# Performance work log

Hardware: AMD Instinct MI355X
Metric: run time of the kernel (lower is better)

The kernel has to match this reference:

```python
import jax, jax.numpy as jnp
import numpy as np

D_MODEL = 512; D_STATE = 64; D_CONV = 4; EXPAND = 1; HEADDIM = 128; NGROUPS = 2; CHUNK = 256
D_INNER = EXPAND * (D_MODEL // 2)          # 256
NHEADS = D_INNER // HEADDIM                 # 2
CONV_DIM = D_INNER + 2 * NGROUPS * D_STATE  # 512
D_IN_PROJ = CONV_DIM + NHEADS               # 514

def silu(x):
    return x * jax.nn.sigmoid(x)

def conv1x1(x, w, b):
    # x: (b,c,h,w), w: (o,c)
    return jnp.einsum('bchw,oc->bohw', x, w) + b[None, :, None, None]

def dwconv3x3(x, w, b):
    # depthwise 3x3, SAME padding; w: (c,1,3,3)
    c = x.shape[1]
    y = jax.lax.conv_general_dilated(x, w, (1, 1), 'SAME', feature_group_count=c,
                                     dimension_numbers=('NCHW', 'OIHW', 'NCHW'))
    return y + b[None, :, None, None]

def causal_dwconv1d(x, w, b):
    # x: (b,L,c); w: (c,k). Torch pads k-1 both sides then slices [:L] -> causal left pad.
    k = w.shape[1]
    xp = jnp.pad(x, ((0, 0), (k - 1, 0), (0, 0))).transpose(0, 2, 1)  # (b,c,L+k-1)
    y = jax.lax.conv_general_dilated(xp, w[:, None, :], (1,), 'VALID',
                                     feature_group_count=w.shape[0],
                                     dimension_numbers=('NCH', 'OIH', 'NCH'))
    return y.transpose(0, 2, 1) + b

def axis_attn(x, qw, qb, fw, fb, axis):
    # DualAxisAggAttn single-axis step
    qkv = conv1x1(x, qw, qb)
    c = x.shape[1]
    q, k, v = qkv[:, :1], qkv[:, 1:1 + c], qkv[:, 1 + c:]
    dim = -1 if axis == 'W' else -2
    scores = jax.nn.softmax(q, axis=dim)
    ctx = jnp.sum(k * scores, axis=dim, keepdims=True)
    out = x + jax.nn.sigmoid(v) * ctx
    return conv1x1(out, fw, fb)

def segsum(x):
    # x: (...,T) -> (...,T,T) lower-triangular segment sums, -inf above diagonal
    T = x.shape[-1]
    cs = jnp.cumsum(x, -1)
    d = cs[..., :, None] - cs[..., None, :]
    mask = jnp.tril(jnp.ones((T, T), bool))
    return jnp.where(mask, d, -jnp.inf)

def ssd(X, A, B, C, chunk):
    # Mamba2 SSD chunked scan. X: (b,l,h,p) = x*dt; A: (b,l,h) = dt*A_head; B,C: (b,l,h,n)
    b, l, h, p = X.shape; n = B.shape[-1]; c = l // chunk
    X = X.reshape(b, c, chunk, h, p)
    B = B.reshape(b, c, chunk, h, n)
    C = C.reshape(b, c, chunk, h, n)
    A = A.reshape(b, c, chunk, h).transpose(0, 3, 1, 2)  # (b,h,c,L)
    Acs = jnp.cumsum(A, -1)
    L = jnp.exp(segsum(A))  # (b,h,c,L,L) intra-chunk decay
    Yd = jnp.einsum('bclhn,bcshn,bhcls,bcshp->bclhp', C, B, L, X)
    dec = jnp.exp(Acs[..., -1:] - Acs)
    st = jnp.einsum('bclhn,bhcl,bclhp->bchpn', B, dec, X)  # chunk end-states
    st = jnp.concatenate([jnp.zeros_like(st[:, :1]), st], 1)
    dchunk = jnp.exp(segsum(jnp.pad(Acs[..., -1], ((0, 0), (0, 0), (1, 0)))))
    st = jnp.einsum('bhzc,bchpn->bzhpn', dchunk, st)[:, :-1]  # states entering each chunk
    Yo = jnp.einsum('bclhn,bchpn,bhcl->bclhp', C, st, jnp.exp(Acs))
    return (Yd + Yo).reshape(b, l, h, p)

def setup_inputs() -> dict:
    key = jax.random.key(0)
    ks = jax.random.split(key, 12)
    s = 0.02
    p = {}
    p['u'] = jax.random.normal(ks[0], (8, D_MODEL, 64, 64), jnp.float32)
    p['sc_w1'] = jax.random.normal(ks[1], (D_MODEL, D_MODEL)) * s
    p['sc_b1'] = jnp.zeros((D_MODEL,))
    p['sc_wdw'] = jax.random.normal(ks[2], (D_MODEL, 1, 3, 3)) * s
    p['sc_bdw'] = jnp.zeros((D_MODEL,))
    p['sc_w2'] = jax.random.normal(ks[3], (D_INNER, D_MODEL)) * s
    p['sc_b2'] = jnp.zeros((D_INNER,))
    p['mc_w'] = jax.random.normal(ks[4], (D_INNER, D_MODEL)) * s
    p['mc_b'] = jnp.zeros((D_INNER,))
    p['qkvW_w'] = jax.random.normal(ks[5], (1 + 2 * D_INNER, D_INNER)) * s
    p['qkvW_b'] = jnp.zeros((1 + 2 * D_INNER,))
    p['qkvH_w'] = jax.random.normal(ks[6], (1 + 2 * D_INNER, D_INNER)) * s
    p['qkvH_b'] = jnp.zeros((1 + 2 * D_INNER,))
    p['fuseW_w'] = jax.random.normal(ks[7], (D_INNER, D_INNER)) * s
    p['fuseW_b'] = jnp.zeros((D_INNER,))
    p['fuseH_w'] = jax.random.normal(ks[8], (D_INNER, D_INNER)) * s
    p['fuseH_b'] = jnp.zeros((D_INNER,))
    p['in_proj_w'] = jax.random.normal(ks[9], (D_IN_PROJ, D_INNER)) * s
    p['conv1d_w'] = jax.random.normal(ks[10], (CONV_DIM, D_CONV)) * s
    p['conv1d_b'] = jnp.zeros((CONV_DIM,))
    dt = np.exp(np.linspace(np.log(1e-3), np.log(0.1), NHEADS))
    p['dt_bias'] = jnp.asarray(dt + np.log(-np.expm1(-dt)), jnp.float32)
    p['A_log'] = jnp.asarray(np.log(np.linspace(1.0, 16.0, NHEADS)), jnp.float32)
    p['D'] = jnp.ones((NHEADS,))
    p['norm_w'] = jnp.ones((D_INNER,))
    p['outp_w'] = jax.random.normal(ks[11], (D_MODEL, 2 * D_INNER)) * s
    p['outp_b'] = jnp.zeros((D_MODEL,))
    return p

def reference(u, sc_w1, sc_b1, sc_wdw, sc_bdw, sc_w2, sc_b2, mc_w, mc_b,
              qkvW_w, qkvW_b, qkvH_w, qkvH_b, fuseW_w, fuseW_b, fuseH_w, fuseH_b,
              in_proj_w, conv1d_w, conv1d_b, dt_bias, A_log, D, norm_w, outp_w, outp_b):
    b, _, H, W = u.shape
    # short_conv branch (light_ConvBlock: 1x1 -> dw3x3 -> 1x1, all SiLU; BN folded into bias)
    z = silu(conv1x1(u, sc_w1, sc_b1))
    z = silu(dwconv3x3(z, sc_wdw, sc_bdw))
    z = silu(conv1x1(z, sc_w2, sc_b2))
    # main branch
    x = silu(conv1x1(u, mc_w, mc_b))
    x = axis_attn(x, qkvW_w, qkvW_b, fuseW_w, fuseW_b, 'W')
    x = axis_attn(x, qkvH_w, qkvH_b, fuseH_w, fuseH_b, 'H')
    seqlen = H * W
    u2 = x.transpose(0, 2, 3, 1).reshape(b, seqlen, D_INNER)  # b (h w) c
    xbcdt = u2 @ in_proj_w.T  # (b,l,d_in_proj)
    xBC = xbcdt[..., :CONV_DIM]
    dt = jax.nn.softplus(xbcdt[..., CONV_DIM:] + dt_bias)  # (b,l,h)
    A = -jnp.exp(A_log)  # (h,)
    xBC = silu(causal_dwconv1d(xBC, conv1d_w, conv1d_b))
    xs = xBC[..., :D_INNER]
    Bs = xBC[..., D_INNER:D_INNER + NGROUPS * D_STATE].reshape(b, seqlen, NGROUPS, D_STATE)
    Cs = xBC[..., D_INNER + NGROUPS * D_STATE:].reshape(b, seqlen, NGROUPS, D_STATE)
    Xh = xs.reshape(b, seqlen, NHEADS, HEADDIM)
    rep = NHEADS // NGROUPS
    Bh = jnp.repeat(Bs, rep, axis=2)
    Ch = jnp.repeat(Cs, rep, axis=2)
    y = ssd(Xh * dt[..., None], dt * A[None, None, :], Bh, Ch, CHUNK)
    y = y + Xh * D[None, None, :, None]  # D skip connection
    y = y.reshape(b, seqlen, D_INNER)
    # RMSNormGated with z=None -> plain RMSNorm
    y = y * jax.lax.rsqrt(jnp.mean(y * y, -1, keepdims=True) + 1e-5) * norm_w
    y = y.reshape(b, H, W, D_INNER).transpose(0, 3, 1, 2)
    y = jnp.concatenate([z, y], axis=1)
    return conv1x1(y, outp_w, outp_b)
```

## Files before the change

### kernel.cpp

```cpp
#include <hip/hip_runtime.h>
#include <hip/hip_bf16.h>
#include <cstddef>
#include <cstdint>

#define PTOT 32768
#define HWSZ 4096

typedef __attribute__((ext_vector_type(8))) short bf16x8;
typedef __attribute__((ext_vector_type(4))) short s16x4;
typedef __attribute__((ext_vector_type(4))) float f32x4;

__device__ __forceinline__ float sigf(float x){ return 1.f/(1.f+__expf(-x)); }
__device__ __forceinline__ float siluf(float x){ return x*sigf(x); }
__device__ __forceinline__ short f2b(float x){
  __hip_bfloat16 h = __float2bfloat16(x);
  return *reinterpret_cast<short*>(&h);
}
__device__ __forceinline__ float b2f(short s){
  unsigned u = ((unsigned)(unsigned short)s) << 16;
  return __uint_as_float(u);
}

__device__ __forceinline__ void gload16(const void* g, void* l){
  __builtin_amdgcn_global_load_lds(
      (const __attribute__((address_space(1))) unsigned int*)g,
      (__attribute__((address_space(3))) unsigned int*)l, 16, 0, 0);
}

__global__ __launch_bounds__(256) void k_cvtw(
    const float* __restrict__ s0, const float* __restrict__ s1, const float* __restrict__ s2,
    const float* __restrict__ s3, const float* __restrict__ s4,
    short* __restrict__ dst){
  int idx = blockIdx.x*256 + threadIdx.x;
  const float* s; int off;
  if      (idx <  262144){ s=s0; off=idx; }
  else if (idx <  393216){ s=s1; off=idx- 262144; }
  else if (idx <  524288){ s=s2; off=idx- 393216; }
  else if (idx <  655616){ s=s3; off=idx- 524288; }
  else if (idx <  917760){ s=s4; off=idx- 655616; }
  else return;
  dst[idx] = f2b(s[off]);
}

__global__ __launch_bounds__(256) void k_wcomp(
    const float* __restrict__ qkvHw, const float* __restrict__ fuWw,
    const float* __restrict__ fuWb,  const float* __restrict__ qkvHb,
    const float* __restrict__ inpw,  const float* __restrict__ fuHw,
    const float* __restrict__ fuHb,
    const float* __restrict__ scb1,  const float* __restrict__ mcb,
    short* __restrict__ wcomb, float* __restrict__ bcomb,
    short* __restrict__ wi2,   float* __restrict__ bi2,
    short* __restrict__ wqH,   short* __restrict__ wdt,
    float* __restrict__ bzx)
{
  int blk = blockIdx.x;
  int tid = threadIdx.x;
  __shared__ float as[256];
  __shared__ float red[256];
  if (blk < 513){
    int i = blk;
    int r = (i==512) ? 0 : (i+1);
    as[tid]  = qkvHw[(size_t)r*256 + tid];
    red[tid] = as[tid] * fuWb[tid];
    __syncthreads();
    for (int off=128; off; off>>=1){ if (tid<off) red[tid]+=red[tid+off]; __syncthreads(); }
    float acc = 0.f;
    #pragma unroll 8
    for (int k=0;k<256;k++) acc += as[k]*fuWw[(size_t)k*256 + tid];
    if (i < 512){
      wcomb[(size_t)(256+i)*256 + tid] = f2b(acc);
      if (tid==0) bcomb[256+i] = red[0] + qkvHb[r];
    } else {
      wqH[tid] = f2b(acc);
      if (tid==0) bcomb[768] = red[0] + qkvHb[0];
    }
  } else if (blk < 769){
    int j = blk - 513;
    wcomb[(size_t)j*256 + tid] = f2b(fuWw[(size_t)j*256 + tid]);
    if (tid==0) bcomb[j] = fuWb[j];
  } else if (blk < 1283){
    int j = blk - 769;
    as[tid]  = inpw[(size_t)j*256 + tid];
    red[tid] = as[tid] * fuHb[tid];
    __syncthreads();
    for (int off=128; off; off>>=1){ if (tid<off) red[tid]+=red[tid+off]; __syncthreads(); }
    float acc = 0.f;
    #pragma unroll 8
    for (int k=0;k<256;k++) acc += as[k]*fuHw[(size_t)k*256 + tid];
    if (j < 512){
      wi2[(size_t)j*256 + tid] = f2b(acc);
      if (tid==0) bi2[j] = red[0];
    } else {
      wdt[(size_t)(j-512)*256 + tid] = f2b(acc);
      if (tid==0) bi2[j] = red[0];
    }
  } else {
    int j = (blk - 1283)*256 + tid;
    bzx[j] = (j < 512) ? scb1[j] : mcb[j-512];
  }
}

__global__ __launch_bounds__(256) void k_transpose(const float* __restrict__ in, short* __restrict__ out){
  __shared__ float tile[64][33];
  int b = blockIdx.z;
  int c0 = blockIdx.y * 64;
  int s0 = blockIdx.x * 32;
  int tx = threadIdx.x, ty = threadIdx.y;
  const float* ip = in + ((size_t)b*512 + c0)*HWSZ + s0;
  for (int i = ty; i < 64; i += 8) tile[i][tx] = ip[(size_t)i*HWSZ + tx];
  __syncthreads();
  for (int i = ty; i < 32; i += 8){
    unsigned lo = (unsigned)(unsigned short)f2b(tile[2*tx][i]);
    unsigned hi = (unsigned)(unsigned short)f2b(tile[2*tx+1][i]);
    unsigned pk = lo | (hi<<16);
    *reinterpret_cast<unsigned*>(&out[((size_t)((b<<12) + s0 + i))*512 + c0 + 2*tx]) = pk;
  }
}

template<int ACT, int OUT_NCHW>
__global__ __launch_bounds__(256) void k_gemm(
    const short* __restrict__ A0, const short* __restrict__ A1,
    int kSplit, int lda0, int lda1,
    const short* __restrict__ Wt, const float* __restrict__ bias,
    void* __restrict__ Cpv, int N, int K, int ldc, int qkvPerm,
    short* __restrict__ Cp2, int nSplit2, int ldc2)
{
  __shared__ short Alds[3][128*32];
  __shared__ short Wlds[2][128*32];

  int tid = threadIdx.x;
  int lane = tid & 63;
  int wv = tid >> 6;
  int wr = wv >> 1, wc = wv & 1;
  int lr = lane & 15, lh = lane >> 4;
  int bm = blockIdx.x * 128;
  int bn = blockIdx.y * 128;

  int rl = lane >> 2;
  int kg = (lane & 3) << 3;

  int ar[2], wnr[2];
  #pragma unroll
  for (int j=0;j<2;j++){
    int r = wv*32 + j*16 + rl;
    ar[j] = bm + r;
    int n = bn + r; if (n > N-1) n = N-1;
    wnr[j] = qkvPerm ? (n+1) : n;
  }

  auto stage_a = [&](int buf, int t){
    int k0 = t << 5;
    #pragma unroll
    for (int j=0;j<2;j++){
      const short* asrc;
      if (k0 < kSplit) asrc = A0 + (size_t)ar[j]*lda0 + (k0 + kg);
      else             asrc = A1 + (size_t)ar[j]*lda1 + (k0 - kSplit + kg);
      gload16(asrc, &Alds[buf][(wv*32 + j*16)*32]);
    }
  };
  auto stage_w = [&](int buf, int t){
    int k0 = t << 5;
    #pragma unroll
    for (int j=0;j<2;j++){
      const short* bsrc = Wt + (size_t)wnr[j]*K + (k0 + kg);
      gload16(bsrc, &Wlds[buf][(wv*32 + j*16)*32]);
    }
  };

  f32x4 acc[4][4];
  #pragma unroll
  for (int i=0;i<4;i++)
    #pragma unroll
    for (int j=0;j<4;j++) acc[i][j] = (f32x4){0.f,0.f,0.f,0.f};

  int NT = K >> 5;
  stage_w(0, 0);
  __builtin_amdgcn_sched_barrier(0);
  stage_a(0, 0);
  __builtin_amdgcn_sched_barrier(0);
  stage_a(1, 1);
  for (int t=0; t<NT; t++){
    int ab = t % 3, wb = t & 1;
    if (t+1 < NT) asm volatile("s_waitcnt vmcnt(2)" ::: "memory");
    else          asm volatile("s_waitcnt vmcnt(0)" ::: "memory");
    __builtin_amdgcn_s_barrier();
    __builtin_amdgcn_sched_barrier(0);
    if (t+1 < NT) stage_w(wb^1, t+1);
    __builtin_amdgcn_sched_barrier(0);
    if (t+2 < NT) stage_a((t+2)%3, t+2);
    __builtin_amdgcn_sched_barrier(0);
    bf16x8 af[4], bfr[4];
    #pragma unroll
    for (int mi=0;mi<4;mi++)
      af[mi] = *reinterpret_cast<const bf16x8*>(&Alds[ab][(wr*64 + mi*16 + lr)*32 + lh*8]);
    #pragma unroll
    for (int ni=0;ni<4;ni++)
      bfr[ni] = *reinterpret_cast<const bf16x8*>(&Wlds[wb][(wc*64 + ni*16 + lr)*32 + lh*8]);
    #pragma unroll
    for (int mi=0;mi<4;mi++)
      #pragma unroll
      for (int ni=0;ni<4;ni++)
        acc[mi][ni] = __builtin_amdgcn_mfma_f32_16x16x32_bf16(af[mi], bfr[ni], acc[mi][ni], 0, 0, 0);
  }

  if (!OUT_NCHW){
    short* Cp = (short*)Cpv;
    #pragma unroll
    for (int mi=0;mi<4;mi++){
      int m = bm + wr*64 + mi*16 + lh*4;
      #pragma unroll
      for (int ni=0;ni<4;ni++){
        int n = bn + wc*64 + ni*16 + lr;
        if (n < N){
          int wn = qkvPerm ? (n+1) : n;
          float bb = bias ? bias[wn] : 0.f;
          #pragma unroll
          for (int r=0;r<4;r++){
            float v = acc[mi][ni][r] + bb;
            if (ACT==1) v = siluf(v);
            short sv = f2b(v);
            if (n < nSplit2) Cp[(size_t)(m+r)*ldc + n] = sv;
            else             Cp2[(size_t)(m+r)*ldc2 + (n - nSplit2)] = sv;
          }
        }
      }
    }
  } else {
    float* Cp = (float*)Cpv;
    float* Sep = ((float*)Alds) + wv*16*68;
    #pragma unroll
    for (int mi=0;mi<4;mi++){
      __syncthreads();
      #pragma unroll
      for (int ni=0;ni<4;ni++){
        int n = bn + wc*64 + ni*16 + lr;
        float bb = (bias && n < N) ? bias[n] : 0.f;
        #pragma unroll
        for (int r=0;r<4;r++){
          float v = acc[mi][ni][r] + bb;
          if (ACT==1) v = siluf(v);
          Sep[(lh*4+r)*68 + ni*16 + lr] = v;
        }
      }
      __syncthreads();
      int m = bm + wr*64 + mi*16 + lr;
      size_t mb = ((size_t)(m>>12)*ldc)*HWSZ + (m & 4095);
      #pragma unroll
      for (int g=0; g<16; g++){
        int nl = g*4 + lh;
        float v = Sep[lr*68 + nl];
        int nn = bn + wc*64 + nl;
        if (nn < N) Cp[mb + (size_t)nn*HWSZ] = v;
      }
    }
  }
}

__global__ __launch_bounds__(256) void k_dwconv3x3(const short* __restrict__ in,
    const float* __restrict__ w, const float* __restrict__ bias, short* __restrict__ out){
  int tid = threadIdx.x;
  int cq = tid & 127;
  int wi = tid >> 7;
  int bw = blockIdx.x;
  int b  = bw >> 5;
  int wc = ((bw & 31) << 1) | wi;
  int h0 = blockIdx.y << 4;
  int c  = cq << 2;

  float arr[36];
  {
    const float* wp = &w[c*9];
    #pragma unroll
    for (int t=0;t<9;t++){
      f32x4 v = *reinterpret_cast<const f32x4*>(wp + t*4);
      arr[t*4+0]=v[0]; arr[t*4+1]=v[1]; arr[t*4+2]=v[2]; arr[t*4+3]=v[3];
    }
  }
  f32x4 bias4 = *reinterpret_cast<const f32x4*>(&bias[c]);

  int pb = b << 12;
  auto ldrow = [&](int r, int dw)->f32x4 {
    int ww = wc + dw;
    if ((unsigned)r >= 64u || (unsigned)ww >= 64u) return (f32x4){0.f,0.f,0.f,0.f};
    s16x4 v = *reinterpret_cast<const s16x4*>(&in[((size_t)(pb + (r<<6) + ww) << 9) + c]);
    return (f32x4){b2f(v[0]), b2f(v[1]), b2f(v[2]), b2f(v[3])};
  };

  f32x4 a00,a01,a02,a10,a11,a12,a20,a21,a22;
  a00=ldrow(h0-1,-1); a01=ldrow(h0-1,0); a02=ldrow(h0-1,1);
  a10=ldrow(h0  ,-1); a11=ldrow(h0  ,0); a12=ldrow(h0  ,1);
  #pragma unroll
  for (int hh=0; hh<16; hh++){
    int h = h0 + hh;
    a20=ldrow(h+1,-1); a21=ldrow(h+1,0); a22=ldrow(h+1,1);
    s16x4 o;
    #pragma unroll
    for (int j=0;j<4;j++){
      float v = bias4[j];
      v = fmaf(a00[j], arr[j*9+0], v);
      v = fmaf(a01[j], arr[j*9+1], v);
      v = fmaf(a02[j], arr[j*9+2], v);
      v = fmaf(a10[j], arr[j*9+3], v);
      v = fmaf(a11[j], arr[j*9+4], v);
      v = fmaf(a12[j], arr[j*9+5], v);
      v = fmaf(a20[j], arr[j*9+6], v);
      v = fmaf(a21[j], arr[j*9+7], v);
      v = fmaf(a22[j], arr[j*9+8], v);
      o[j] = f2b(siluf(v));
    }
    *reinterpret_cast<s16x4*>(&out[((size_t)(pb + (h<<6) + wc) << 9) + c]) = o;
    a00=a10; a01=a11; a02=a12;
    a10=a20; a11=a21; a12=a22;
  }
}

__global__ __launch_bounds__(256) void k_attn_ctx(
    const short* __restrict__ xq, int xqld, const short* __restrict__ wq, const float* __restrict__ bq,
    const short* __restrict__ qkv, int qld, int kOff,
    float* __restrict__ ctx, int axisH){
  int bl = blockIdx.x;
  int b = bl >> 6, line = bl & 63;
  int tid = threadIdx.x;
  int pbase = b << 12;
  __shared__ float qs[64], es[64];
  __shared__ float qpart[4][64];
  __shared__ float part[8][260];
  auto pos = [&](int t)->int { return axisH ? (pbase | (t<<6) | line) : (pbase | (line<<6) | t); };
  {
    int t = tid & 63, qr = tid >> 6;
    const short* xp = &xq[(size_t)pos(t)*xqld + qr*64];
    const short* wp = &wq[qr*64];
    float pq = 0.f;
    #pragma unroll
    for (int j=0;j<8;j++){
      bf16x8 xv = *reinterpret_cast<const bf16x8*>(xp + j*8);
      bf16x8 wv = *reinterpret_cast<const bf16x8*>(wp + j*8);
      #pragma unroll
      for (int e=0;e<8;e++) pq = fmaf(b2f(xv[e]), b2f(wv[e]), pq);
    }
    qpart[qr][t] = pq;
  }
  __syncthreads();
  if (tid < 64) qs[tid] = bq[0] + qpart[0][tid] + qpart[1][tid] + qpart[2][tid] + qpart[3][tid];
  __syncthreads();
  float mx = -1e30f;
  for (int t=0;t<64;t++) mx = fmaxf(mx, qs[t]);
  if (tid < 64) es[tid] = __expf(qs[tid]-mx);
  __syncthreads();
  int tg = tid >> 5;
  int cg = tid & 31;
  float pacc[8];
  #pragma unroll
  for (int j=0;j<8;j++) pacc[j]=0.f;
  #pragma unroll
  for (int tt=0; tt<8; tt++){
    int t = tg*8 + tt;
    bf16x8 kv = *reinterpret_cast<const bf16x8*>(&qkv[(size_t)pos(t)*qld + kOff + cg*8]);
    float e = es[t];
    #pragma unroll
    for (int j=0;j<8;j++) pacc[j] = fmaf(e, b2f(kv[j]), pacc[j]);
  }
  #pragma unroll
  for (int j=0;j<8;j++) part[tg][cg*8+j] = pacc[j];
  __syncthreads();
  float s = 0.f;
  for (int t=0;t<64;t++) s += es[t];
  float inv = 1.f/s;
  int c = tid;
  float v = 0.f;
  #pragma unroll
  for (int g=0; g<8; g++) v += part[g][c];
  ctx[(size_t)bl*256 + c] = v*inv;
}

__global__ __launch_bounds__(256) void k_attn_apply(const short* __restrict__ x, int xld,
    const short* __restrict__ qkv, int qld, int vOff, const float* __restrict__ ctx,
    short* __restrict__ out, int axisH){
  int idx = blockIdx.x*256 + threadIdx.x;
  int p = idx >> 5;
  int c0 = (idx & 31) << 3;
  int line = axisH ? (p & 63) : ((p >> 6) & 63);
  int bl = (p >> 12)*64 + line;
  bf16x8 vv = *reinterpret_cast<const bf16x8*>(&qkv[(size_t)p*qld + vOff + c0]);
  bf16x8 xv = *reinterpret_cast<const bf16x8*>(&x[(size_t)p*xld + c0]);
  const float* cp = &ctx[(size_t)bl*256 + c0];
  bf16x8 o;
  #pragma unroll
  for (int j=0;j<8;j++)
    o[j] = f2b(b2f(xv[j]) + sigf(b2f(vv[j]))*cp[j]);
  *reinterpret_cast<bf16x8*>(&out[(size_t)p*256 + c0]) = o;
}

__global__ __launch_bounds__(256) void k_dt(const short* __restrict__ xwh,
    const short* __restrict__ wdt, const float* __restrict__ bdt,
    const float* __restrict__ dt_bias, float* __restrict__ dtb){
  int tid = threadIdx.x, lane = tid & 63, wv = tid >> 6;
  int p = blockIdx.x*4 + wv;
  s16x4 xv = *reinterpret_cast<const s16x4*>(&xwh[(size_t)p*256 + lane*4]);
  s16x4 w0 = *reinterpret_cast<const s16x4*>(&wdt[lane*4]);
  s16x4 w1 = *reinterpret_cast<const s16x4*>(&wdt[256 + lane*4]);
  float d0 = 0.f, d1 = 0.f;
  #pragma unroll
  for (int j=0;j<4;j++){
    float xf = b2f(xv[j]);
    d0 = fmaf(xf, b2f(w0[j]), d0);
    d1 = fmaf(xf, b2f(w1[j]), d1);
  }
  #pragma unroll
  for (int off=32; off; off>>=1){ d0 += __shfl_down(d0, off); d1 += __shfl_down(d1, off); }
  if (lane == 0){
    float x0 = d0 + bdt[0] + dt_bias[0];
    float x1 = d1 + bdt[1] + dt_bias[1];
    dtb[(size_t)p*2 + 0] = (x0 > 20.f) ? x0 : log1pf(__expf(x0));
    dtb[(size_t)p*2 + 1] = (x1 > 20.f) ? x1 : log1pf(__expf(x1));
  }
}

__global__ __launch_bounds__(256) void k_conv1d(const short* __restrict__ xbc_in,
    const float* __restrict__ w, const float* __restrict__ bias, short* __restrict__ xBC){
  int tid = threadIdx.x;
  int cq = tid & 127;
  int c  = cq << 2;
  int half = tid >> 7;
  int bs = blockIdx.x;
  int b  = bs >> 7;
  int t0 = ((((bs & 127) << 1) | half) << 4);

  float wk[16];
  {
    const float* wp = &w[c*4];
    #pragma unroll
    for (int t=0;t<4;t++){
      f32x4 v = *reinterpret_cast<const f32x4*>(wp + t*4);
      wk[t*4+0]=v[0]; wk[t*4+1]=v[1]; wk[t*4+2]=v[2]; wk[t*4+3]=v[3];
    }
  }
  f32x4 bias4 = *reinterpret_cast<const f32x4*>(&bias[c]);

  int pb = b << 12;
  auto ld = [&](int t)->f32x4 {
    if (t < 0) return (f32x4){0.f,0.f,0.f,0.f};
    s16x4 v = *reinterpret_cast<const s16x4*>(&xbc_in[((size_t)(pb + t) << 9) + c]);
    return (f32x4){b2f(v[0]), b2f(v[1]), b2f(v[2]), b2f(v[3])};
  };

  f32x4 x0,x1,x2,x3;
  x0 = ld(t0-3); x1 = ld(t0-2); x2 = ld(t0-1);
  #pragma unroll
  for (int tt=0; tt<16; tt++){
    int t = t0 + tt;
    x3 = ld(t);
    s16x4 o;
    #pragma unroll
    for (int j=0;j<4;j++){
      float v = bias4[j];
      v = fmaf(x0[j], wk[j*4+0], v);
      v = fmaf(x1[j], wk[j*4+1], v);
      v = fmaf(x2[j], wk[j*4+2], v);
      v = fmaf(x3[j], wk[j*4+3], v);
      o[j] = f2b(siluf(v));
    }
    *reinterpret_cast<s16x4*>(&xBC[((size_t)(pb + t) << 9) + c]) = o;
    x0=x1; x1=x2; x2=x3;
  }
}

__global__ __launch_bounds__(256) void k_ssd_states(
  const short* __restrict__ xBC, const float* __restrict__ dtb, const float* __restrict__ A_log,
  float* __restrict__ states, float* __restrict__ AcsG, float* __restrict__ AtotG)
{
  int ci = blockIdx.x, h = blockIdx.y, b = blockIdx.z;
  int tid = threadIdx.x, lane = tid & 63, wv = tid >> 6;
  int lg = lane >> 4, lr = lane & 15;
  __shared__ float sa[256], sb[256];
  __shared__ short Bt[64*72];
  __shared__ short Xt[128*72];
  int base = (b<<12) | (ci<<8);
  float Ah = -__expf(A_log[h]);
  sa[tid] = dtb[(size_t)(base + tid)*2 + h] * Ah;
  __syncthreads();
  float* src = sa; float* dst = sb;
  for (int off=1; off<256; off<<=1){
    float v = src[tid];
    if (tid >= off) v += src[tid - off];
    dst[tid] = v;
    __syncthreads();
    float* tswap = src; src = dst; dst = tswap;
  }
  float acs = src[tid];
  float atot = src[255];
  AcsG[((size_t)((b*2+h)*16 + ci))*256 + tid] = acs;
  if (tid == 0) AtotG[(b*2+h)*16 + ci] = atot;

  f32x4 acc[8];
  #pragma unroll
  for (int pf=0;pf<8;pf++) acc[pf] = (f32x4){0.f,0.f,0.f,0.f};

  for (int t0=0; t0<256; t0+=64){
    __syncthreads();
    {
      int t = tid >> 2;
      int n0 = (tid & 3) << 4;
      float d = __expf(atot - src[t0 + t]);
      const short* sp = &xBC[(size_t)(base + t0 + t)*512 + 256 + (h<<6) + n0];
      bf16x8 v0 = *reinterpret_cast<const bf16x8*>(sp);
      bf16x8 v1 = *reinterpret_cast<const bf16x8*>(sp+8);
      #pragma unroll
      for (int e=0;e<8;e++) Bt[(n0+e)*72 + t]   = f2b(b2f(v0[e])*d);
      #pragma unroll
      for (int e=0;e<8;e++) Bt[(n0+8+e)*72 + t] = f2b(b2f(v1[e])*d);
    }
    {
      int t = tid >> 2;
      int p0 = (tid & 3) << 5;
      float dtv = dtb[(size_t)(base + t0 + t)*2 + h];
      const short* sp = &xBC[(size_t)(base + t0 + t)*512 + (h<<7) + p0];
      #pragma unroll
      for (int q=0;q<4;q++){
        bf16x8 v = *reinterpret_cast<const bf16x8*>(sp + q*8);
        #pragma unroll
        for (int e=0;e<8;e++) Xt[(p0 + q*8 + e)*72 + t] = f2b(b2f(v[e])*dtv);
      }
    }
    __syncthreads();
    #pragma unroll
    for (int kk=0; kk<2; kk++){
      bf16x8 af = *reinterpret_cast<const bf16x8*>(&Bt[(wv*16 + lr)*72 + kk*32 + lg*8]);
      #pragma unroll
      for (int pf=0;pf<8;pf++){
        bf16x8 xf = *reinterpret_cast<const bf16x8*>(&Xt[(pf*16 + lr)*72 + kk*32 + lg*8]);
        acc[pf] = __builtin_amdgcn_mfma_f32_16x16x32_bf16(af, xf, acc[pf], 0, 0, 0);
      }
    }
  }
  float* stp = states + (((size_t)(b*16+ci)*2 + h) << 13);
  #pragma unroll
  for (int pf=0;pf<8;pf++){
    #pragma unroll
    for (int r=0;r<4;r++)
      stp[(wv*16 + lg*4 + r)*128 + pf*16 + lr] = acc[pf][r];
  }
}

__global__ __launch_bounds__(256) void k_ssd_scan(const float* __restrict__ states,
    const float* __restrict__ AtotG, float* __restrict__ R){
  int bh = blockIdx.x;
  int b = bh >> 1, h = bh & 1;
  int tid = threadIdx.x;
  float r[32];
  #pragma unroll
  for (int j=0;j<32;j++) r[j]=0.f;
  for (int ci=0; ci<16; ci++){
    size_t off = (((size_t)(b*16+ci)*2) + h) << 13;
    #pragma unroll
    for (int j=0;j<32;j++) R[off + tid + (j<<8)] = r[j];
    if (ci < 15){
      float sc = __expf(AtotG[bh*16 + ci]);
      #pragma unroll
      for (int j=0;j<32;j++) r[j] = fmaf(sc, r[j], states[off + tid + (j<<8)]);
    }
  }
}

__global__ __launch_bounds__(256) void k_ssd_y_norm(
  const short* __restrict__ xBC, const float* __restrict__ dtb,
  const float* __restrict__ AcsG, const float* __restrict__ R,
  const float* __restrict__ Dp, const float* __restrict__ nw, short* __restrict__ ynorm)
{
  int bx = blockIdx.x;
  int ci = bx >> 2, lt = bx & 3;
  int b = blockIdx.y;
  int tid = threadIdx.x, lane = tid & 63, w = tid >> 6;
  int lg = lane >> 4, lr = lane & 15;
  int base = (b<<12) | (ci<<8);
  int l0 = lt << 6;

  __shared__ short Cbf[64*72];
  __shared__ short Bbf[64*72];
  __shared__ short Xt [128*76];
  __shared__ short Sbf[64*72];
  __shared__ float acs_l[64], acs_s[64], dt_s[64];

  auto body = [&](int h, f32x4* yv){
    __syncthreads();
    const float* acsrow = AcsG + ((size_t)((b*2+h)*16 + ci))*256;
    {
      int row = tid >> 2, c0 = (tid & 3) << 4;
      const short* src = &xBC[(size_t)(base + l0 + row)*512 + 384 + (h<<6) + c0];
      *reinterpret_cast<bf16x8*>(&Cbf[row*72 + c0])     = *reinterpret_cast<const bf16x8*>(src);
      *reinterpret_cast<bf16x8*>(&Cbf[row*72 + c0 + 8]) = *reinterpret_cast<const bf16x8*>(src+8);
    }
    if (tid < 64) acs_l[tid] = acsrow[l0 + tid];

    f32x4 yacc[8];
    #pragma unroll
    for (int pf=0;pf<8;pf++) yacc[pf] = (f32x4){0.f,0.f,0.f,0.f};

    for (int s0 = 0; s0 <= l0; s0 += 64){
      __syncthreads();
      {
        int row = tid >> 2, c0 = (tid & 3) << 4;
        const short* src = &xBC[(size_t)(base + s0 + row)*512 + 256 + (h<<6) + c0];
        *reinterpret_cast<bf16x8*>(&Bbf[row*72 + c0])     = *reinterpret_cast<const bf16x8*>(src);
        *reinterpret_cast<bf16x8*>(&Bbf[row*72 + c0 + 8]) = *reinterpret_cast<const bf16x8*>(src+8);
      }
      {
        int s = tid >> 2;
        int p0 = (tid & 3) << 5;
        const short* src = &xBC[(size_t)(base + s0 + s)*512 + (h<<7) + p0];
        #pragma unroll
        for (int q=0;q<4;q++){
          bf16x8 v = *reinterpret_cast<const bf16x8*>(src + q*8);
          #pragma unroll
          for (int e=0;e<8;e++) Xt[(p0 + q*8 + e)*76 + s] = v[e];
        }
      }
      if (tid < 64){
        acs_s[tid] = acsrow[s0 + tid];
        dt_s[tid]  = dtb[(size_t)(base + s0 + tid)*2 + h];
      }
      __syncthreads();

      f32x4 sacc[4];
      #pragma unroll
      for (int f=0;f<4;f++) sacc[f] = (f32x4){0.f,0.f,0.f,0.f};
      bf16x8 ca0 = *reinterpret_cast<const bf16x8*>(&Cbf[(w*16+lr)*72 + lg*8]);
      bf16x8 ca1 = *reinterpret_cast<const bf16x8*>(&Cbf[(w*16+lr)*72 + 32 + lg*8]);
      #pragma unroll
      for (int f=0;f<4;f++){
        bf16x8 bb0 = *reinterpret_cast<const bf16x8*>(&Bbf[(f*16+lr)*72 + lg*8]);
        bf16x8 bb1 = *reinterpret_cast<const bf16x8*>(&Bbf[(f*16+lr)*72 + 32 + lg*8]);
        sacc[f] = __builtin_amdgcn_mfma_f32_16x16x32_bf16(ca0, bb0, sacc[f], 0, 0, 0);
        sacc[f] = __builtin_amdgcn_mfma_f32_16x16x32_bf16(ca1, bb1, sacc[f], 0, 0, 0);
      }
      #pragma unroll
      for (int f=0;f<4;f++){
        #pragma unroll
        for (int r=0;r<4;r++){
          int ll = w*16 + lg*4 + r;
          int ss = f*16 + lr;
          float v = 0.f;
          if (s0 + ss <= l0 + ll)
            v = sacc[f][r] * __expf(acs_l[ll] - acs_s[ss]) * dt_s[ss];
          Sbf[ll*72 + ss] = f2b(v);
        }
      }
      __syncthreads();

      bf16x8 sa0 = *reinterpret_cast<const bf16x8*>(&Sbf[(w*16+lr)*72 + lg*8]);
      bf16x8 sa1 = *reinterpret_cast<const bf16x8*>(&Sbf[(w*16+lr)*72 + 32 + lg*8]);
      #pragma unroll
      for (int pf=0;pf<8;pf++){
        bf16x8 x0 = *reinterpret_cast<const bf16x8*>(&Xt[(pf*16+lr)*76 + lg*8]);
        bf16x8 x1 = *reinterpret_cast<const bf16x8*>(&Xt[(pf*16+lr)*76 + 32 + lg*8]);
        yacc[pf] = __builtin_amdgcn_mfma_f32_16x16x32_bf16(sa0, x0, yacc[pf], 0, 0, 0);
        yacc[pf] = __builtin_amdgcn_mfma_f32_16x16x32_bf16(sa1, x1, yacc[pf], 0, 0, 0);
      }
    }

    __syncthreads();
    {
      size_t roff = (((size_t)(b*16+ci)*2) + h) << 13;
      int n = tid >> 2;
      const float* src = R + roff + (size_t)n*128;
      #pragma unroll
      for (int j=0;j<8;j++){
        int p = ((tid & 3) << 2) + (j << 4);
        float4 f = *reinterpret_cast<const float4*>(&src[p]);
        Xt[(p+0)*76 + n] = f2b(f.x);
        Xt[(p+1)*76 + n] = f2b(f.y);
        Xt[(p+2)*76 + n] = f2b(f.z);
        Xt[(p+3)*76 + n] = f2b(f.w);
      }
    }
    __syncthreads();
    f32x4 racc[8];
    #pragma unroll
    for (int pf=0;pf<8;pf++) racc[pf] = (f32x4){0.f,0.f,0.f,0.f};
    {
      bf16x8 ca0 = *reinterpret_cast<const bf16x8*>(&Cbf[(w*16+lr)*72 + lg*8]);
      bf16x8 ca1 = *reinterpret_cast<const bf16x8*>(&Cbf[(w*16+lr)*72 + 32 + lg*8]);
      #pragma unroll
      for (int pf=0;pf<8;pf++){
        bf16x8 x0 = *reinterpret_cast<const bf16x8*>(&Xt[(pf*16+lr)*76 + lg*8]);
        bf16x8 x1 = *reinterpret_cast<const bf16x8*>(&Xt[(pf*16+lr)*76 + 32 + lg*8]);
        racc[pf] = __builtin_amdgcn_mfma_f32_16x16x32_bf16(ca0, x0, racc[pf], 0, 0, 0);
        racc[pf] = __builtin_amdgcn_mfma_f32_16x16x32_bf16(ca1, x1, racc[pf], 0, 0, 0);
      }
    }
    float Dh = Dp[h];
    float el[4];
    #pragma unroll
    for (int r=0;r<4;r++) el[r] = __expf(acs_l[w*16 + lg*4 + r]);
    #pragma unroll
    for (int pf=0;pf<8;pf++){
      f32x4 o;
      #pragma unroll
      for (int r=0;r<4;r++){
        int ll = w*16 + lg*4 + r;
        int p = pf*16 + lr;
        size_t pix = (size_t)(base + l0 + ll);
        float xraw = b2f(xBC[pix*512 + (h<<7) + p]);
        o[r] = yacc[pf][r] + el[r]*racc[pf][r] + Dh*xraw;
      }
      yv[pf] = o;
    }
  };

  f32x4 y0[8], y1[8];
  body(0, y0);
  body(1, y1);

  f32x4 ss = (f32x4){0.f,0.f,0.f,0.f};
  #pragma unroll
  for (int pf=0;pf<8;pf++){
    #pragma unroll
    for (int r=0;r<4;r++)
      ss[r] += y0[pf][r]*y0[pf][r] + y1[pf][r]*y1[pf][r];
  }
  #pragma unroll
  for (int m=1; m<16; m<<=1){
    #pragma unroll
    for (int r=0;r<4;r++) ss[r] += __shfl_xor(ss[r], m);
  }
  f32x4 scale;
  #pragma unroll
  for (int r=0;r<4;r++) scale[r] = rsqrtf(ss[r]*(1.f/256.f) + 1e-5f);

  #pragma unroll
  for (int pf=0;pf<8;pf++){
    float nw0 = nw[pf*16 + lr];
    float nw1 = nw[128 + pf*16 + lr];
    #pragma unroll
    for (int r=0;r<4;r++){
      size_t pix = (size_t)(base + l0 + w*16 + lg*4 + r);
      ynorm[pix*256 + pf*16 + lr]        = f2b(y0[pf][r]*scale[r]*nw0);
      ynorm[pix*256 + 128 + pf*16 + lr]  = f2b(y1[pf][r]*scale[r]*nw1);
    }
  }
}

extern "C" void kernel_launch(void* const* d_in, const int* in_sizes, int n_in,
                              void* d_out, int out_size, void* d_ws, size_t ws_size,
                              hipStream_t stream)
{
  (void)in_sizes; (void)n_in; (void)out_size; (void)ws_size;
  const float* u        = (const float*)d_in[0];
  const float* sc_w1    = (const float*)d_in[1];
  const float* sc_b1    = (const float*)d_in[2];
  const float* sc_wdw   = (const float*)d_in[3];
  const float* sc_bdw   = (const float*)d_in[4];
  const float* sc_w2    = (const float*)d_in[5];
  const float* sc_b2    = (const float*)d_in[6];
  const float* mc_w     = (const float*)d_in[7];
  const float* mc_b     = (const float*)d_in[8];
  const float* qkvW_w   = (const float*)d_in[9];
  const float* qkvW_b   = (const float*)d_in[10];
  const float* qkvH_w   = (const float*)d_in[11];
  const float* qkvH_b   = (const float*)d_in[12];
  const float* fuseW_w  = (const float*)d_in[13];
  const float* fuseW_b  = (const float*)d_in[14];
  const float* fuseH_w  = (const float*)d_in[15];
  const float* fuseH_b  = (const float*)d_in[16];
  const float* in_proj_w= (const float*)d_in[17];
  const float* conv1d_w = (const float*)d_in[18];
  const float* conv1d_b = (const float*)d_in[19];
  const float* dt_bias  = (const float*)d_in[20];
  const float* A_log    = (const float*)d_in[21];
  const float* Dp       = (const float*)d_in[22];
  const float* norm_w   = (const float*)d_in[23];
  const float* outp_w   = (const float*)d_in[24];
  const float* outp_b   = (const float*)d_in[25];

  char* wsb = (char*)d_ws;
  size_t off = 0;
  auto alloc = [&](size_t bytes){ void* p = wsb + off; off = (off + bytes + 255) & ~(size_t)255; return p; };
  short* wbf   = (short*)alloc((size_t)1247000*2);
  float* bcomb = (float*)alloc(769*4);
  float* bi2   = (float*)alloc(514*4);
  float* bzx   = (float*)alloc(768*4);
  short* slotB = (short*)alloc((size_t)PTOT*768*2);
  short* slotC = (short*)alloc((size_t)PTOT*512*2);
  short* slotZ = (short*)alloc((size_t)PTOT*256*2);
  short* slotE = (short*)alloc((size_t)PTOT*256*2);
  short* slotF = (short*)alloc((size_t)PTOT*256*2);
  float* slotS = (float*)alloc((size_t)4460000*4);

  float* dtb     = slotS;
  float* AcsG    = slotS + 65536;
  float* AtotG   = slotS + 131072;
  float* statesB = slotS + 131328;
  float* Rb      = slotS + 131328 + 2097152;
  float* ctxb    = slotS;
  short* ynorm   = slotE;
  short* xwh     = slotF;

  short* w_zx   = wbf + 0;
  short* w_sc2  = wbf + 393216;
  short* w_qkvW = wbf + 524288;
  short* w_outp = wbf + 655616;
  short* wcomb  = wbf + 917760;
  short* wi2    = wbf + 1114368;
  short* wqH    = wbf + 1245440;
  short* wdt    = wbf + 1245696;

  short* u_pm = (short*)d_out;
  float* out  = (float*)d_out;

  const int BIG = 1<<30;

  k_cvtw<<<3585, 256, 0, stream>>>(sc_w1, mc_w, sc_w2, qkvW_w, outp_w, wbf);
  k_wcomp<<<1286, 256, 0, stream>>>(qkvH_w, fuseW_w, fuseW_b, qkvH_b, in_proj_w, fuseH_w, fuseH_b,
                                    sc_b1, mc_b, wcomb, bcomb, wi2, bi2, wqH, wdt, bzx);
  k_transpose<<<dim3(128,8,8), dim3(32,8), 0, stream>>>(u, u_pm);

  k_gemm<1,0><<<dim3(256,6), 256, 0, stream>>>(u_pm, u_pm, BIG, 512, 512, w_zx, bzx,
                                               slotB, 768, 512, 512, 0, slotE, 512, 256);
  k_dwconv3x3<<<dim3(256,4), 256, 0, stream>>>(slotB, sc_wdw, sc_bdw, slotC);
  k_gemm<1,0><<<dim3(256,2), 256, 0, stream>>>(slotC, slotC, BIG, 512, 512, w_sc2, sc_b2,
                                               slotZ, 256, 512, 256, 0, nullptr, BIG, 0);

  k_gemm<0,0><<<dim3(256,4), 256, 0, stream>>>(slotE, slotE, BIG, 256, 256, w_qkvW, qkvW_b,
                                               slotB, 512, 256, 512, 1, nullptr, BIG, 0);
  k_attn_ctx<<<512, 256, 0, stream>>>(slotE, 256, w_qkvW, qkvW_b, slotB, 512, 0, ctxb, 0);
  k_attn_apply<<<4096, 256, 0, stream>>>(slotE, 256, slotB, 512, 256, ctxb, xwh, 0);
  k_gemm<0,0><<<dim3(256,6), 256, 0, stream>>>(xwh, xwh, BIG, 256, 256, wcomb, bcomb,
                                               slotB, 768, 256, 768, 0, nullptr, BIG, 0);
  k_attn_ctx<<<512, 256, 0, stream>>>(xwh, 256, wqH, bcomb + 768, slotB, 768, 256, ctxb, 1);
  k_attn_apply<<<4096, 256, 0, stream>>>(slotB, 768, slotB, 768, 512, ctxb, xwh, 1);
  k_gemm<0,0><<<dim3(256,4), 256, 0, stream>>>(xwh, xwh, BIG, 256, 256, wi2, bi2,
                                               slotB, 512, 256, 512, 0, nullptr, BIG, 0);
  k_dt<<<8192, 256, 0, stream>>>(xwh, wdt, bi2 + 512, dt_bias, dtb);
  k_conv1d<<<1024, 256, 0, stream>>>(slotB, conv1d_w, conv1d_b, slotC);

  k_ssd_states<<<dim3(16,2,8), 256, 0, stream>>>(slotC, dtb, A_log, statesB, AcsG, AtotG);
  k_ssd_scan<<<16, 256, 0, stream>>>(statesB, AtotG, Rb);
  k_ssd_y_norm<<<dim3(64,8), 256, 0, stream>>>(slotC, dtb, AcsG, Rb, Dp, norm_w, ynorm);

  k_gemm<0,1><<<dim3(256,4), 256, 0, stream>>>(slotZ, ynorm, 256, 256, 256, w_outp, outp_b,
                                               out, 512, 512, 512, 0, nullptr, BIG, 0);
}
```

Before: 420.3 us.

## Replace multi-stage LDS pipeline in GEMM with single-buffered loop

Removes the triple/double-buffered async staging of A and W tiles and replaces it with a simple per-iteration load, barrier, compute, barrier loop on a single LDS buffer. Base pointers are precomputed per row. Shared memory shrinks to one 17KB arena, which may allow more resident blocks per CU. In exchange, global loads no longer overlap with MFMA work, and each k-step now has an extra barrier.

```diff
diff --git a/kernel.cpp b/kernel.cpp
--- a/kernel.cpp
+++ b/kernel.cpp
@@ -125,8 +125,9 @@
     void* __restrict__ Cpv, int N, int K, int ldc, int qkvPerm,
     short* __restrict__ Cp2, int nSplit2, int ldc2)
 {
-  __shared__ short Alds[3][128*32];
-  __shared__ short Wlds[2][128*32];
+  __shared__ char arena[17408];
+  short* Alds = (short*)arena;
+  short* Wlds = (short*)(arena + 8192);
 
   int tid = threadIdx.x;
   int lane = tid & 63;
@@ -139,33 +140,19 @@
   int rl = lane >> 2;
   int kg = (lane & 3) << 3;
 
-  int ar[2], wnr[2];
+  const short* aB0[2];
+  const short* aB1[2];
+  const short* wB[2];
   #pragma unroll
   for (int j=0;j<2;j++){
     int r = wv*32 + j*16 + rl;
-    ar[j] = bm + r;
+    int m = bm + r;
+    aB0[j] = A0 + (size_t)m*lda0 + kg;
+    aB1[j] = A1 + (size_t)m*lda1 + kg;
     int n = bn + r; if (n > N-1) n = N-1;
-    wnr[j] = qkvPerm ? (n+1) : n;
-  }
-
-  auto stage_a = [&](int buf, int t){
-    int k0 = t << 5;
-    #pragma unroll
-    for (int j=0;j<2;j++){
-      const short* asrc;
-      if (k0 < kSplit) asrc = A0 + (size_t)ar[j]*lda0 + (k0 + kg);
-      else             asrc = A1 + (size_t)ar[j]*lda1 + (k0 - kSplit + kg);
-      gload16(asrc, &Alds[buf][(wv*32 + j*16)*32]);
-    }
-  };
-  auto stage_w = [&](int buf, int t){
-    int k0 = t << 5;
-    #pragma unroll
-    for (int j=0;j<2;j++){
-      const short* bsrc = Wt + (size_t)wnr[j]*K + (k0 + kg);
-      gload16(bsrc, &Wlds[buf][(wv*32 + j*16)*32]);
-    }
-  };
+    int wn = qkvPerm ? (n+1) : n;
+    wB[j] = Wt + (size_t)wn*K + kg;
+  }
 
   f32x4 acc[4][4];
   #pragma unroll
@@ -173,34 +160,31 @@
     #pragma unroll
     for (int j=0;j<4;j++) acc[i][j] = (f32x4){0.f,0.f,0.f,0.f};
 
-  int NT = K >> 5;
-  stage_w(0, 0);
-  __builtin_amdgcn_sched_barrier(0);
-  stage_a(0, 0);
-  __builtin_amdgcn_sched_barrier(0);
-  stage_a(1, 1);
-  for (int t=0; t<NT; t++){
-    int ab = t % 3, wb = t & 1;
-    if (t+1 < NT) asm volatile("s_waitcnt vmcnt(2)" ::: "memory");
-    else          asm volatile("s_waitcnt vmcnt(0)" ::: "memory");
-    __builtin_amdgcn_s_barrier();
-    __builtin_amdgcn_sched_barrier(0);
-    if (t+1 < NT) stage_w(wb^1, t+1);
-    __builtin_amdgcn_sched_barrier(0);
-    if (t+2 < NT) stage_a((t+2)%3, t+2);
-    __builtin_amdgcn_sched_barrier(0);
+  for (int k0 = 0; k0 < K; k0 += 32){
+    {
+      const short* s0;
+      const short* s1;
+      if (k0 < kSplit){ s0 = aB0[0] + k0; s1 = aB0[1] + k0; }
+      else            { s0 = aB1[0] + (k0 - kSplit); s1 = aB1[1] + (k0 - kSplit); }
+      gload16(s0, &Alds[(wv*32)*32]);
+      gload16(s1, &Alds[(wv*32 + 16)*32]);
+      gload16(wB[0] + k0, &Wlds[(wv*32)*32]);
+      gload16(wB[1] + k0, &Wlds[(wv*32 + 16)*32]);
+    }
+    __syncthreads();
     bf16x8 af[4], bfr[4];
     #pragma unroll
     for (int mi=0;mi<4;mi++)
-      af[mi] = *reinterpret_cast<const bf16x8*>(&Alds[ab][(wr*64 + mi*16 + lr)*32 + lh*8]);
+      af[mi] = *reinterpret_cast<const bf16x8*>(&Alds[(wr*64 + mi*16 + lr)*32 + lh*8]);
     #pragma unroll
     for (int ni=0;ni<4;ni++)
-      bfr[ni] = *reinterpret_cast<const bf16x8*>(&Wlds[wb][(wc*64 + ni*16 + lr)*32 + lh*8]);
+      bfr[ni] = *reinterpret_cast<const bf16x8*>(&Wlds[(wc*64 + ni*16 + lr)*32 + lh*8]);
     #pragma unroll
     for (int mi=0;mi<4;mi++)
       #pragma unroll
       for (int ni=0;ni<4;ni++)
         acc[mi][ni] = __builtin_amdgcn_mfma_f32_16x16x32_bf16(af[mi], bfr[ni], acc[mi][ni], 0, 0, 0);
+    __syncthreads();
   }
 
   if (!OUT_NCHW){
@@ -227,7 +211,7 @@
     }
   } else {
     float* Cp = (float*)Cpv;
-    float* Sep = ((float*)Alds) + wv*16*68;
+    float* Sep = ((float*)arena) + wv*16*68;
     #pragma unroll
     for (int mi=0;mi<4;mi++){
       __syncthreads();
```

Result: slower. 468.3 us (median of 5 runs) (+11.4%).
